# Performance work log

Hardware: AMD Instinct MI355X
Metric: run time of the kernel (lower is better)

Reference implementation:

```python
import jax, jax.numpy as jnp
import numpy as np

N = 6144       # num nodes
F_IN = 256     # in_channels
HID = 64       # hidden
OUT = 64       # out_channels
E = 196608     # num edges (avg degree 32)
ALPHA = 0.8
EPS = 1e-6     # prob clamp (stand-in for torch clamp_probs tiny)
BN_EPS = 1e-5


def setup_inputs() -> dict:
    key = jax.random.key(0)
    ks = jax.random.split(key, 6)
    x = jax.random.normal(ks[0], (N, F_IN), jnp.float32)
    edge_index = jax.random.randint(ks[1], (2, E), 0, N, dtype=jnp.int64)
    W1 = jax.random.normal(ks[2], (F_IN, HID), jnp.float32) / np.float32(np.sqrt(F_IN))
    b1 = jnp.zeros((HID,), jnp.float32)
    W2 = jax.random.normal(ks[3], (HID, OUT), jnp.float32) / np.float32(np.sqrt(HID))
    b2 = jnp.zeros((OUT,), jnp.float32)
    gamma = jnp.ones((HID,), jnp.float32)
    beta = jnp.zeros((HID,), jnp.float32)
    prelu_a = jnp.full((1,), 0.25, jnp.float32)
    u = jax.random.uniform(ks[4], (N, N), jnp.float32, minval=1e-6, maxval=1.0 - 1e-6)
    return dict(x=x, edge_index=edge_index, W1=W1, b1=b1, W2=W2, b2=b2,
                gamma=gamma, beta=beta, prelu_a=prelu_a, u=u)


def _gcn_edge(x, src, dst, W, b, n):
    # PyG GCNConv: add self-loops, D^-1/2 (A+I) D^-1/2 (x W) + b
    h = x @ W
    loop = jnp.arange(n, dtype=src.dtype)
    src2 = jnp.concatenate([src, loop])
    dst2 = jnp.concatenate([dst, loop])
    deg = jax.ops.segment_sum(jnp.ones_like(src2, h.dtype), dst2, num_segments=n)
    dinv = jax.lax.rsqrt(deg)  # deg >= 1 due to self-loops
    norm = dinv[src2] * dinv[dst2]
    out = jax.ops.segment_sum(h[src2] * norm[:, None], dst2, num_segments=n)
    return out + b


def reference(x, edge_index, W1, b1, W2, b2, gamma, beta, prelu_a, u):
    n = x.shape[0]
    src, dst = edge_index[0], edge_index[1]

    # --- sample(alpha=0.8, x, edge_index) ---
    h = _gcn_edge(x, src, dst, W1, b1, n)                      # conv1 on original graph
    adj_orig = jnp.zeros((n, n), h.dtype).at[src, dst].set(1.0)  # directed scatter, as in the loop
    adj_logits = h @ h.T                                        # [N, N]
    edge_probs = ALPHA * (adj_logits / jnp.max(adj_logits)) + (1.0 - ALPHA) * adj_orig
    edge_probs = jnp.maximum(edge_probs, 0.0)                   # where(p<0, 0, p)
    p = jnp.clip(edge_probs, EPS, 1.0 - EPS)
    logits = jnp.log(p) - jnp.log1p(-p)
    noise = jnp.log(u) - jnp.log1p(-u)                          # logistic noise
    soft = jax.nn.sigmoid(logits + noise)                       # RelaxedBernoulli, temperature=1
    st = soft + jax.lax.stop_gradient(jnp.round(soft) - soft)   # straight-through hard sample
    a = jnp.triu(st, 1)
    a = a + a.T
    eye = jnp.eye(n, dtype=a.dtype)
    adj_sampled = a + eye                                       # fill_diagonal_(1) (triu(1) zeroed diag)

    # --- main conv stack on sampled graph (nonzero -> edge list -> GCNConv adds self-loops again) ---
    A = adj_sampled + eye                                       # diag weight becomes 2, faithful to PyG
    dinv = jax.lax.rsqrt(A.sum(axis=1))
    An = dinv[:, None] * A * dinv[None, :]
    x1 = An @ (x @ W1) + b1                                     # conv 0
    z = jnp.where(x1 >= 0, x1, prelu_a * x1)                    # PReLU
    mean = x1.mean(axis=0)
    var = x1.var(axis=0)                                        # biased, training-mode BN
    xb = gamma * (x1 - mean) * jax.lax.rsqrt(var + BN_EPS) + beta
    xr = jax.nn.relu(xb)                                        # dropout p=0 is a no-op
    x2 = An @ (xr @ W2) + b2                                    # conv 1
    return (x2, z, adj_sampled, adj_logits, adj_orig)
```

## Files before the change

kernel.cpp:

```cpp
#include <hip/hip_runtime.h>
#include <math.h>

#define NN 6144
#define FIN 256
#define HID 64
#define NW 96
typedef unsigned long long u64;


__global__ __launch_bounds__(256) void k_hxw(const float* __restrict__ x,
                                             const float* __restrict__ W1,
                                             double* __restrict__ hxw) {
  int t = blockIdx.x * 256 + threadIdx.x;
  int i = t >> 6, c = t & 63;
  const float* xr = x + (size_t)i * FIN;
  double a = 0.0;
#pragma unroll 8
  for (int k = 0; k < FIN; ++k)
    a = fma((double)xr[k], (double)W1[k * HID + c], a);
  hxw[t] = a;
}

__global__ __launch_bounds__(256) void k_edges(const int* __restrict__ ei, int E,
                                               int* __restrict__ deg,
                                               u64* __restrict__ bitO) {
  int e = blockIdx.x * 256 + threadIdx.x;
  if (e >= E) return;
  int s = ei[e], d = ei[E + e];
  atomicAdd(&deg[d], 1);
  atomicOr(&bitO[(size_t)s * NW + (d >> 6)], 1ull << (d & 63));
}

__global__ __launch_bounds__(256) void k_dinv(const int* __restrict__ deg,
                                              double* __restrict__ dinv) {
  int i = blockIdx.x * 256 + threadIdx.x;
  if (i < NN) dinv[i] = 1.0 / sqrt((double)(deg[i] + 1));
}

__global__ __launch_bounds__(256) void k_agg(const int* __restrict__ ei, int E,
                                             const double* __restrict__ hxw,
                                             const double* __restrict__ dinv,
                                             double* __restrict__ hagg) {
  int t = blockIdx.x * 256 + threadIdx.x;
  if (t >= E * HID) return;
  int e = t >> 6, c = t & 63;
  int s = ei[e], d = ei[E + e];
  atomicAdd(&hagg[(size_t)d * HID + c], hxw[(size_t)s * HID + c] * (dinv[s] * dinv[d]));
}

__global__ __launch_bounds__(256) void k_selfbias(const double* __restrict__ hxw,
                                                  const double* __restrict__ dinv,
                                                  const float* __restrict__ b1,
                                                  double* __restrict__ hagg) {
  int t = blockIdx.x * 256 + threadIdx.x;
  int i = t >> 6, c = t & 63;
  hagg[t] += hxw[t] * dinv[i] * dinv[i] + (double)b1[c];
}

__global__ __launch_bounds__(256) void k_lmax(const double* __restrict__ h,
                                              u64* __restrict__ lmax) {
  __shared__ double red[256];
  int i = blockIdx.x * 256 + threadIdx.x;
  const double* hr = h + (size_t)i * HID;
  double s = 0.0;
  for (int c = 0; c < HID; ++c) s = fma(hr[c], hr[c], s);
  red[threadIdx.x] = s;
  __syncthreads();
  for (int w = 128; w > 0; w >>= 1) {
    if (threadIdx.x < w) {
      double o = red[threadIdx.x + w];
      if (o > red[threadIdx.x]) red[threadIdx.x] = o;
    }
    __syncthreads();
  }
  if (threadIdx.x == 0)
    atomicMax(lmax, (u64)__double_as_longlong(red[0]));
}

#define FMA16D(A0, A1, A2, A3, C0, C1, C2, C3)                                   \
  acc[0][0] = fma(A0, C0, acc[0][0]); acc[0][1] = fma(A0, C1, acc[0][1]);        \
  acc[0][2] = fma(A0, C2, acc[0][2]); acc[0][3] = fma(A0, C3, acc[0][3]);        \
  acc[1][0] = fma(A1, C0, acc[1][0]); acc[1][1] = fma(A1, C1, acc[1][1]);        \
  acc[1][2] = fma(A1, C2, acc[1][2]); acc[1][3] = fma(A1, C3, acc[1][3]);        \
  acc[2][0] = fma(A2, C0, acc[2][0]); acc[2][1] = fma(A2, C1, acc[2][1]);        \
  acc[2][2] = fma(A2, C2, acc[2][2]); acc[2][3] = fma(A2, C3, acc[2][3]);        \
  acc[3][0] = fma(A3, C0, acc[3][0]); acc[3][1] = fma(A3, C1, acc[3][1]);        \
  acc[3][2] = fma(A3, C2, acc[3][2]); acc[3][3] = fma(A3, C3, acc[3][3]);

__global__ __launch_bounds__(256) void k_tile(const double* __restrict__ h,
                                              const u64* __restrict__ lmaxp,
                                              const float* __restrict__ u,
                                              const u64* __restrict__ bitO,
                                              float* __restrict__ adjL,
                                              float* __restrict__ adjS,
                                              float* __restrict__ adjO,
                                              u64* __restrict__ bitT) {
  int I = blockIdx.y, J = blockIdx.x;
  if (J < I) return;
  __shared__ __align__(16) double smem[2 * 64 * 34];
  double* As = smem;
  double* Bs = smem + 64 * 34;
  float* Ls = (float*)smem;
  float* Ss = ((float*)smem) + 64 * 68;
  int t = threadIdx.x;
  int tx = t & 15, ty = t >> 4;
  double acc[4][4];
#pragma unroll
  for (int p = 0; p < 4; ++p)
#pragma unroll
    for (int q = 0; q < 4; ++q) acc[p][q] = 0.0;
  const double* hI = h + (size_t)I * 64 * HID;
  const double* hJ = h + (size_t)J * 64 * HID;
  for (int k0 = 0; k0 < 64; k0 += 32) {
    __syncthreads();
    for (int idx = t; idx < 1024; idx += 256) {
      int r = idx >> 4, k2 = (idx & 15) << 1;
      *(double2*)&As[r * 34 + k2] = *(const double2*)&hI[r * 64 + k0 + k2];
      *(double2*)&Bs[r * 34 + k2] = *(const double2*)&hJ[r * 64 + k0 + k2];
    }
    __syncthreads();
#pragma unroll 8
    for (int k = 0; k < 32; k += 2) {
      double2 A0 = *(const double2*)&As[ty * 34 + k];
      double2 A1 = *(const double2*)&As[(ty + 16) * 34 + k];
      double2 A2 = *(const double2*)&As[(ty + 32) * 34 + k];
      double2 A3 = *(const double2*)&As[(ty + 48) * 34 + k];
      double2 C0 = *(const double2*)&Bs[tx * 34 + k];
      double2 C1 = *(const double2*)&Bs[(tx + 16) * 34 + k];
      double2 C2 = *(const double2*)&Bs[(tx + 32) * 34 + k];
      double2 C3 = *(const double2*)&Bs[(tx + 48) * 34 + k];
      FMA16D(A0.x, A1.x, A2.x, A3.x, C0.x, C1.x, C2.x, C3.x)
      FMA16D(A0.y, A1.y, A2.y, A3.y, C0.y, C1.y, C2.y, C3.y)
    }
  }
  __syncthreads();
  double Lmax = __longlong_as_double((long long)(*lmaxp));
  bool diag = (I == J);
#pragma unroll
  for (int p = 0; p < 4; ++p) {
    int r = ty + 16 * p;
    int gi = I * 64 + r;
    u64 wO = bitO[(size_t)gi * NW + J];
    float sv[4];
#pragma unroll
    for (int q = 0; q < 4; ++q) {
      int c = tx + 16 * q;
      int gj = J * 64 + c;
      double L = acc[p][q];
      float lf = (float)L;
      adjL[(size_t)gi * NN + gj] = lf;
      adjO[(size_t)gi * NN + gj] = (float)((wO >> c) & 1ull);
      float stv;
      if (diag && r == c) {
        stv = 1.0f;
      } else {
        int ga = gi < gj ? gi : gj, gb = gi < gj ? gj : gi;
        size_t ab = (size_t)ga * NN + gb;
        double uu = (double)u[ab];
        double ao = (double)(int)((bitO[(size_t)ga * NW + (gb >> 6)] >> (gb & 63)) & 1ull);
        double ep = 0.8 * (L / Lmax) + 0.2 * ao;
        if (ep < 0.0) ep = 0.0;
        double pl = ep;
        if (pl < 1e-6) pl = 1e-6;
        double hi = 1.0 - 1e-6;
        if (pl > hi) pl = hi;
        stv = (pl > 1.0 - uu) ? 1.0f : 0.0f;
      }
      sv[q] = stv;
      adjS[(size_t)gi * NN + gj] = stv;
      if (!diag) {
        Ls[c * 68 + r] = lf;
        Ss[c * 68 + r] = stv;
      }
    }
    u64 word = 0;
#pragma unroll
    for (int q = 0; q < 4; ++q) {
      u64 m = __ballot(sv[q] > 0.5f);
      word |= ((m >> ((ty & 3) * 16)) & 0xFFFFull) << (16 * q);
    }
    if (tx == 0) bitT[(size_t)J * NN + gi] = word;
  }
  if (!diag) {
    __syncthreads();
    for (int i4 = t; i4 < 1024; i4 += 256) {
      int a = i4 >> 4, b4 = (i4 & 15) << 2;
      int grow = J * 64 + a;
      size_t off = (size_t)grow * NN + (I * 64 + b4);
      *(float4*)(adjL + off) = *(const float4*)&Ls[a * 68 + b4];
      *(float4*)(adjS + off) = *(const float4*)&Ss[a * 68 + b4];
      u64 wOm = bitO[(size_t)grow * NW + I];
      *(float4*)(adjO + off) = make_float4((float)((wOm >> b4) & 1ull),
                                           (float)((wOm >> (b4 + 1)) & 1ull),
                                           (float)((wOm >> (b4 + 2)) & 1ull),
                                           (float)((wOm >> (b4 + 3)) & 1ull));
    }
    for (int k2 = 0; k2 < 16; ++k2) {
      int idx = t + (k2 << 8);
      int a = idx >> 6, b = idx & 63;
      u64 m = __ballot(Ss[a * 68 + b] > 0.5f);
      if ((t & 63) == 0) bitT[(size_t)I * NN + (J * 64 + a)] = m;
    }
  }
}

__global__ __launch_bounds__(256) void k_rowsumB(const u64* __restrict__ bitT,
                                                 double* __restrict__ dinv2) {
  int i = blockIdx.x * 256 + threadIdx.x;
  int cnt = 0;
#pragma unroll
  for (int J = 0; J < NW; ++J) cnt += __popcll(bitT[(size_t)J * NN + i]);
  dinv2[i] = 1.0 / sqrt((double)(cnt + 1));
}

__global__ __launch_bounds__(256) void k_gscale(const double* __restrict__ hv,
                                                const double* __restrict__ dinv2,
                                                float* __restrict__ g) {
  int t = blockIdx.x * 256 + threadIdx.x;
  int j = t >> 6;
  g[t] = (float)(dinv2[j] * hv[t]);
}

#define FMA16F(A0, A1, A2, A3, CV)                                                   \
  acc[0][0] = fmaf(A0, CV.x, acc[0][0]); acc[0][1] = fmaf(A0, CV.y, acc[0][1]);      \
  acc[0][2] = fmaf(A0, CV.z, acc[0][2]); acc[0][3] = fmaf(A0, CV.w, acc[0][3]);      \
  acc[1][0] = fmaf(A1, CV.x, acc[1][0]); acc[1][1] = fmaf(A1, CV.y, acc[1][1]);      \
  acc[1][2] = fmaf(A1, CV.z, acc[1][2]); acc[1][3] = fmaf(A1, CV.w, acc[1][3]);      \
  acc[2][0] = fmaf(A2, CV.x, acc[2][0]); acc[2][1] = fmaf(A2, CV.y, acc[2][1]);      \
  acc[2][2] = fmaf(A2, CV.z, acc[2][2]); acc[2][3] = fmaf(A2, CV.w, acc[2][3]);      \
  acc[3][0] = fmaf(A3, CV.x, acc[3][0]); acc[3][1] = fmaf(A3, CV.y, acc[3][1]);      \
  acc[3][2] = fmaf(A3, CV.z, acc[3][2]); acc[3][3] = fmaf(A3, CV.w, acc[3][3]);

__global__ __launch_bounds__(256) void k_anmm(const u64* __restrict__ bitT,
                                              const float* __restrict__ g,
                                              float* __restrict__ accb) {
  int I = blockIdx.x;
  int s = blockIdx.y;
  __shared__ __align__(16) float as[64 * 68];
  __shared__ __align__(16) float gs[64 * 64];
  int t = threadIdx.x, tx = t & 15, ty = t >> 4;
  float acc[4][4];
#pragma unroll
  for (int p = 0; p < 4; ++p)
#pragma unroll
    for (int q = 0; q < 4; ++q) acc[p][q] = 0.0f;
  for (int Jt = s * 12; Jt < (s + 1) * 12; ++Jt) {
    __syncthreads();
    for (int i4 = t; i4 < 1024; i4 += 256) {
      int r = i4 >> 4, c4 = (i4 & 15) << 2;
      *(float4*)&gs[r * 64 + c4] = *(const float4*)&g[(size_t)(Jt * 64 + r) * HID + c4];
    }
    for (int idx = t; idx < 4096; idx += 256) {
      int r = idx >> 6, cc = idx & 63;
      u64 w = bitT[(size_t)Jt * NN + I * 64 + r];
      as[r * 68 + cc] = (float)((w >> cc) & 1ull);
    }
    __syncthreads();
#pragma unroll 2
    for (int j0 = 0; j0 < 64; j0 += 4) {
      float4 a0v = *(const float4*)&as[ty * 68 + j0];
      float4 a1v = *(const float4*)&as[(ty + 16) * 68 + j0];
      float4 a2v = *(const float4*)&as[(ty + 32) * 68 + j0];
      float4 a3v = *(const float4*)&as[(ty + 48) * 68 + j0];
      float4 cv0 = *(const float4*)&gs[j0 * 64 + (tx << 2)];
      float4 cv1 = *(const float4*)&gs[(j0 + 1) * 64 + (tx << 2)];
      float4 cv2 = *(const float4*)&gs[(j0 + 2) * 64 + (tx << 2)];
      float4 cv3 = *(const float4*)&gs[(j0 + 3) * 64 + (tx << 2)];
      FMA16F(a0v.x, a1v.x, a2v.x, a3v.x, cv0)
      FMA16F(a0v.y, a1v.y, a2v.y, a3v.y, cv1)
      FMA16F(a0v.z, a1v.z, a2v.z, a3v.z, cv2)
      FMA16F(a0v.w, a1v.w, a2v.w, a3v.w, cv3)
    }
  }
  float* out = accb + (size_t)s * NN * HID;
#pragma unroll
  for (int p = 0; p < 4; ++p) {
    float4 v = make_float4(acc[p][0], acc[p][1], acc[p][2], acc[p][3]);
    *(float4*)&out[(size_t)(I * 64 + ty + 16 * p) * HID + (tx << 2)] = v;
  }
}

__global__ __launch_bounds__(256) void k_ep1(const float* __restrict__ accb,
                                             const float* __restrict__ g,
                                             const double* __restrict__ dinv2,
                                             const float* __restrict__ b1,
                                             const float* __restrict__ prelu,
                                             float* __restrict__ x1,
                                             float* __restrict__ zout) {
  int t = blockIdx.x * 256 + threadIdx.x;
  int i = t >> 6, c = t & 63;
  double ss = 0.0;
  for (int s = 0; s < 8; ++s) ss += (double)accb[(size_t)s * NN * HID + t];
  float v = (float)(dinv2[i] * (ss + (double)g[t])) + b1[c];
  x1[t] = v;
  float pa = prelu[0];
  zout[t] = v >= 0.0f ? v : pa * v;
}

__global__ __launch_bounds__(256) void k_bnstats(const float* __restrict__ x1,
                                                 double* __restrict__ meanv,
                                                 double* __restrict__ istd) {
  __shared__ double r1[256], r2[256];
  int c = blockIdx.x;
  double s1 = 0.0, s2 = 0.0;
  for (int i = threadIdx.x; i < NN; i += 256) {
    double v = (double)x1[(size_t)i * HID + c];
    s1 += v;
    s2 += v * v;
  }
  r1[threadIdx.x] = s1;
  r2[threadIdx.x] = s2;
  __syncthreads();
  for (int w = 128; w > 0; w >>= 1) {
    if (threadIdx.x < w) {
      r1[threadIdx.x] += r1[threadIdx.x + w];
      r2[threadIdx.x] += r2[threadIdx.x + w];
    }
    __syncthreads();
  }
  if (threadIdx.x == 0) {
    double m = r1[0] / (double)NN;
    double var = r2[0] / (double)NN - m * m;
    meanv[c] = m;
    istd[c] = 1.0 / sqrt(var + 1e-5);
  }
}

__global__ __launch_bounds__(256) void k_xryg2(const float* __restrict__ x1,
                                               const double* __restrict__ meanv,
                                               const double* __restrict__ istd,
                                               const float* __restrict__ gamma,
                                               const float* __restrict__ beta,
                                               const float* __restrict__ W2,
                                               const double* __restrict__ dinv2,
                                               float* __restrict__ g2) {
  __shared__ float xs[4 * 64];
  int t = threadIdx.x;
  int t2 = blockIdx.x * 256 + t;
  int c = t & 63;
  float v = gamma[c] * (float)(((double)x1[t2] - meanv[c]) * istd[c]) + beta[c];
  xs[t] = v > 0.0f ? v : 0.0f;
  __syncthreads();
  const float* xrow = xs + (t >> 6) * 64;
  float a = 0.0f;
#pragma unroll 8
  for (int k = 0; k < HID; ++k) a = fmaf(xrow[k], W2[k * HID + c], a);
  int j = t2 >> 6;
  g2[t2] = (float)(dinv2[j] * (double)a);
}

__global__ __launch_bounds__(256) void k_ep2(const float* __restrict__ accb,
                                             const float* __restrict__ g2,
                                             const double* __restrict__ dinv2,
                                             const float* __restrict__ b2p,
                                             float* __restrict__ x2out) {
  int t = blockIdx.x * 256 + threadIdx.x;
  int i = t >> 6, c = t & 63;
  double ss = 0.0;
  for (int s = 0; s < 8; ++s) ss += (double)accb[(size_t)s * NN * HID + t];
  x2out[t] = (float)(dinv2[i] * (ss + (double)g2[t])) + b2p[c];
}

extern "C" void kernel_launch(void* const* d_in, const int* in_sizes, int n_in,
                              void* d_out, int out_size, void* d_ws, size_t ws_size,
                              hipStream_t stream) {
  const float* x = (const float*)d_in[0];
  const int* ei = (const int*)d_in[1];
  const float* W1 = (const float*)d_in[2];
  const float* b1 = (const float*)d_in[3];
  const float* W2 = (const float*)d_in[4];
  const float* b2 = (const float*)d_in[5];
  const float* gamma = (const float*)d_in[6];
  const float* beta = (const float*)d_in[7];
  const float* prelu = (const float*)d_in[8];
  const float* u = (const float*)d_in[9];
  int E = in_sizes[1] / 2;

  float* out = (float*)d_out;
  float* o_x2 = out;
  float* o_z = out + (size_t)NN * HID;
  float* o_adjS = out + (size_t)2 * NN * HID;
  float* o_adjL = o_adjS + (size_t)NN * NN;
  float* o_adjO = o_adjL + (size_t)NN * NN;

  char* w = (char*)d_ws;
  double* hxw = (double*)w;
  double* hagg = (double*)(w + 3145728);
  double* dinv = (double*)(w + 6291456);
  int* deg = (int*)(w + 6340608);
  float* accb = (float*)w;
  double* dinv2 = (double*)(w + 12582912);
  u64* lmax = (u64*)(w + 12632064);
  double* meanv = (double*)(w + 12632128);
  double* istd = (double*)(w + 12632640);
  float* x1 = (float*)(w + 12633152);
  float* gg = (float*)(w + 14206016);
  float* g2 = (float*)(w + 17351744);
  u64* bitO = (u64*)(w + 12633152);
  u64* bitT = (u64*)(w + 18924608);

  hipMemsetAsync(deg, 0, NN * sizeof(int), stream);
  hipMemsetAsync(hagg, 0, (size_t)NN * HID * sizeof(double), stream);
  hipMemsetAsync(lmax, 0, sizeof(u64), stream);
  hipMemsetAsync(bitO, 0, (size_t)NN * NW * sizeof(u64), stream);

  k_hxw<<<NN * HID / 256, 256, 0, stream>>>(x, W1, hxw);
  k_edges<<<(E + 255) / 256, 256, 0, stream>>>(ei, E, deg, bitO);
  k_dinv<<<NN / 256, 256, 0, stream>>>(deg, dinv);
  k_agg<<<(E * HID + 255) / 256, 256, 0, stream>>>(ei, E, hxw, dinv, hagg);
  k_selfbias<<<NN * HID / 256, 256, 0, stream>>>(hxw, dinv, b1, hagg);
  k_lmax<<<NN / 256, 256, 0, stream>>>(hagg, lmax);
  dim3 gt(96, 96);
  k_tile<<<gt, 256, 0, stream>>>(hagg, lmax, u, bitO, o_adjL, o_adjS, o_adjO, bitT);
  k_rowsumB<<<NN / 256, 256, 0, stream>>>(bitT, dinv2);
  k_gscale<<<NN * HID / 256, 256, 0, stream>>>(hxw, dinv2, gg);
  dim3 ga(96, 8);
  k_anmm<<<ga, 256, 0, stream>>>(bitT, gg, accb);
  k_ep1<<<NN * HID / 256, 256, 0, stream>>>(accb, gg, dinv2, b1, prelu, x1, o_z);
  k_bnstats<<<HID, 256, 0, stream>>>(x1, meanv, istd);
  k_xryg2<<<NN * HID / 256, 256, 0, stream>>>(x1, meanv, istd, gamma, beta, W2, dinv2, g2);
  k_anmm<<<ga, 256, 0, stream>>>(bitT, g2, accb);
  k_ep2<<<NN * HID / 256, 256, 0, stream>>>(accb, g2, dinv2, b2, o_x2);
}
```

Measured before the change: 1.046 ms.

## Fuse small elementwise kernels and decode adjacency bits in registers in k_anmm

Merges the self-loop/bias add into the row-max reduction kernel and the row-degree count into the g-scaling kernel, which removes two launches and a pass over the data. In the sampled-adjacency matmul, each thread now keeps its four 64-bit bitmask words in registers and extracts bits inline, replacing the shared-memory float expansion of the adjacency tile. This saves shared memory and one pass per tile, but adds shift/convert instructions to the inner loop. The fused per-row kernels use one thread per row with strided access, so their memory coalescing is worse than before.

```diff
diff --git a/kernel.cpp b/kernel.cpp
--- a/kernel.cpp
+++ b/kernel.cpp
@@ -48,22 +48,22 @@
   atomicAdd(&hagg[(size_t)d * HID + c], hxw[(size_t)s * HID + c] * (dinv[s] * dinv[d]));
 }
 
-__global__ __launch_bounds__(256) void k_selfbias(const double* __restrict__ hxw,
-                                                  const double* __restrict__ dinv,
-                                                  const float* __restrict__ b1,
-                                                  double* __restrict__ hagg) {
-  int t = blockIdx.x * 256 + threadIdx.x;
-  int i = t >> 6, c = t & 63;
-  hagg[t] += hxw[t] * dinv[i] * dinv[i] + (double)b1[c];
-}
-
-__global__ __launch_bounds__(256) void k_lmax(const double* __restrict__ h,
-                                              u64* __restrict__ lmax) {
+__global__ __launch_bounds__(256) void k_sblmax(const double* __restrict__ hxw,
+                                                const double* __restrict__ dinv,
+                                                const float* __restrict__ b1,
+                                                double* __restrict__ hagg,
+                                                u64* __restrict__ lmax) {
   __shared__ double red[256];
   int i = blockIdx.x * 256 + threadIdx.x;
-  const double* hr = h + (size_t)i * HID;
+  double di = dinv[i];
+  double* hr = hagg + (size_t)i * HID;
+  const double* xr = hxw + (size_t)i * HID;
   double s = 0.0;
-  for (int c = 0; c < HID; ++c) s = fma(hr[c], hr[c], s);
+  for (int c = 0; c < HID; ++c) {
+    double v = hr[c] + (xr[c] * di * di + (double)b1[c]);
+    hr[c] = v;
+    s = fma(v, v, s);
+  }
   red[threadIdx.x] = s;
   __syncthreads();
   for (int w = 128; w > 0; w >>= 1) {
@@ -204,21 +204,19 @@
   }
 }
 
-__global__ __launch_bounds__(256) void k_rowsumB(const u64* __restrict__ bitT,
-                                                 double* __restrict__ dinv2) {
+__global__ __launch_bounds__(256) void k_rsg(const u64* __restrict__ bitT,
+                                             const double* __restrict__ hv,
+                                             double* __restrict__ dinv2,
+                                             float* __restrict__ g) {
   int i = blockIdx.x * 256 + threadIdx.x;
   int cnt = 0;
 #pragma unroll
   for (int J = 0; J < NW; ++J) cnt += __popcll(bitT[(size_t)J * NN + i]);
-  dinv2[i] = 1.0 / sqrt((double)(cnt + 1));
-}
-
-__global__ __launch_bounds__(256) void k_gscale(const double* __restrict__ hv,
-                                                const double* __restrict__ dinv2,
-                                                float* __restrict__ g) {
-  int t = blockIdx.x * 256 + threadIdx.x;
-  int j = t >> 6;
-  g[t] = (float)(dinv2[j] * hv[t]);
+  double di = 1.0 / sqrt((double)(cnt + 1));
+  dinv2[i] = di;
+  const double* hr = hv + (size_t)i * HID;
+  float* gr = g + (size_t)i * HID;
+  for (int c = 0; c < HID; ++c) gr[c] = (float)(di * hr[c]);
 }
 
 #define FMA16F(A0, A1, A2, A3, CV)                                                   \
@@ -236,7 +234,6 @@
                                               float* __restrict__ accb) {
   int I = blockIdx.x;
   int s = blockIdx.y;
-  __shared__ __align__(16) float as[64 * 68];
   __shared__ __align__(16) float gs[64 * 64];
   int t = threadIdx.x, tx = t & 15, ty = t >> 4;
   float acc[4][4];
@@ -250,26 +247,20 @@
       int r = i4 >> 4, c4 = (i4 & 15) << 2;
       *(float4*)&gs[r * 64 + c4] = *(const float4*)&g[(size_t)(Jt * 64 + r) * HID + c4];
     }
-    for (int idx = t; idx < 4096; idx += 256) {
-      int r = idx >> 6, cc = idx & 63;
-      u64 w = bitT[(size_t)Jt * NN + I * 64 + r];
-      as[r * 68 + cc] = (float)((w >> cc) & 1ull);
-    }
-    __syncthreads();
-#pragma unroll 2
-    for (int j0 = 0; j0 < 64; j0 += 4) {
-      float4 a0v = *(const float4*)&as[ty * 68 + j0];
-      float4 a1v = *(const float4*)&as[(ty + 16) * 68 + j0];
-      float4 a2v = *(const float4*)&as[(ty + 32) * 68 + j0];
-      float4 a3v = *(const float4*)&as[(ty + 48) * 68 + j0];
-      float4 cv0 = *(const float4*)&gs[j0 * 64 + (tx << 2)];
-      float4 cv1 = *(const float4*)&gs[(j0 + 1) * 64 + (tx << 2)];
-      float4 cv2 = *(const float4*)&gs[(j0 + 2) * 64 + (tx << 2)];
-      float4 cv3 = *(const float4*)&gs[(j0 + 3) * 64 + (tx << 2)];
-      FMA16F(a0v.x, a1v.x, a2v.x, a3v.x, cv0)
-      FMA16F(a0v.y, a1v.y, a2v.y, a3v.y, cv1)
-      FMA16F(a0v.z, a1v.z, a2v.z, a3v.z, cv2)
-      FMA16F(a0v.w, a1v.w, a2v.w, a3v.w, cv3)
+    const u64* bw = bitT + (size_t)Jt * NN + I * 64;
+    u64 w0 = bw[ty];
+    u64 w1 = bw[ty + 16];
+    u64 w2 = bw[ty + 32];
+    u64 w3 = bw[ty + 48];
+    __syncthreads();
+#pragma unroll 8
+    for (int j = 0; j < 64; ++j) {
+      float4 cv = *(const float4*)&gs[j * 64 + (tx << 2)];
+      float b0 = (float)((w0 >> j) & 1ull);
+      float b1 = (float)((w1 >> j) & 1ull);
+      float b2 = (float)((w2 >> j) & 1ull);
+      float b3 = (float)((w3 >> j) & 1ull);
+      FMA16F(b0, b1, b2, b3, cv)
     }
   }
   float* out = accb + (size_t)s * NN * HID;
@@ -408,12 +399,10 @@
   k_edges<<<(E + 255) / 256, 256, 0, stream>>>(ei, E, deg, bitO);
   k_dinv<<<NN / 256, 256, 0, stream>>>(deg, dinv);
   k_agg<<<(E * HID + 255) / 256, 256, 0, stream>>>(ei, E, hxw, dinv, hagg);
-  k_selfbias<<<NN * HID / 256, 256, 0, stream>>>(hxw, dinv, b1, hagg);
-  k_lmax<<<NN / 256, 256, 0, stream>>>(hagg, lmax);
+  k_sblmax<<<NN / 256, 256, 0, stream>>>(hxw, dinv, b1, hagg, lmax);
   dim3 gt(96, 96);
   k_tile<<<gt, 256, 0, stream>>>(hagg, lmax, u, bitO, o_adjL, o_adjS, o_adjO, bitT);
-  k_rowsumB<<<NN / 256, 256, 0, stream>>>(bitT, dinv2);
-  k_gscale<<<NN * HID / 256, 256, 0, stream>>>(hxw, dinv2, gg);
+  k_rsg<<<NN / 256, 256, 0, stream>>>(bitT, hxw, dinv2, gg);
   dim3 ga(96, 8);
   k_anmm<<<ga, 256, 0, stream>>>(bitT, gg, accb);
   k_ep1<<<NN * HID / 256, 256, 0, stream>>>(accb, gg, dinv2, b1, prelu, x1, o_z);
```

New measurement: 1.207 ms. +15.4%, slower.
